# Kernel tuning notes

Measured on AMD Instinct MI355X. Metric: run time of the kernel, lower is better.

The kernel has to match this reference:

```python
import jax, jax.numpy as jnp
import numpy as np

# Module hyperparameters (match init_kwargs)
T0, Z0, T1, Z1, K, S, ROUTING = 4, 16, 8, 16, 5, 1, 3
PAD = 2  # hard-coded padding=2 in the torch module
N, H, W_SP = 4, 128, 128


def setup_inputs() -> dict:
    key = jax.random.key(0)
    k1, k2 = jax.random.split(key)
    u = jax.random.normal(k1, (N, T0, Z0, H, W_SP), dtype=jnp.float32)
    # t_0 independent Conv2d(z_0 -> t_1*z_1, k, s, padding=2, bias=False) weights
    W = jax.random.normal(k2, (T0, T1 * Z1, Z0, K, K), dtype=jnp.float32) * 0.05
    return {"u": u, "W": W}


def _squash(p):
    # squash along last (z_1) axis, matching torch: p_norm = sqrt(|p|^2 + 1e-9)
    n2 = jnp.sum(p * p, axis=-1, keepdims=True)
    n = jnp.sqrt(n2 + 1e-9)
    return n2 / (1.0 + n2) * p / n


def _capsule_convs(u, W):
    # t_0 independent convs == one grouped conv with feature_group_count=t_0
    n, t0, z0, h, w = u.shape
    x = u.reshape(n, t0 * z0, h, w)
    wk = W.reshape(t0 * T1 * Z1, z0, K, K)
    y = jax.lax.conv_general_dilated(
        x, wk, window_strides=(S, S), padding=[(PAD, PAD), (PAD, PAD)],
        dimension_numbers=("NCHW", "OIHW", "NCHW"), feature_group_count=t0)
    h1, w1 = y.shape[2], y.shape[3]
    # [N, t0*t1*z1, H1, W1] -> u_hat [t0, N, H1, W1, t1, z1]
    y = y.reshape(n, t0, T1, Z1, h1, w1)
    return jnp.transpose(y, (1, 0, 4, 5, 2, 3))


def _routing(u_hat):
    t0, n, h, w, t1, z1 = u_hat.shape
    dt = u_hat.dtype
    b = jnp.zeros((t0, n, t1, h, w), dt)  # NCHW layout per capsule type
    neg_inf = jnp.array(-jnp.inf, dt)
    zero = jnp.array(0.0, dt)
    win = (1, 1, 1, K, K)
    ones = (1, 1, 1, 1, 1)
    pad = [(0, 0), (0, 0), (0, 0), (PAD, PAD), (PAD, PAD)]
    v = None
    for d in range(ROUTING):
        uh = jax.lax.stop_gradient(u_hat) if d < ROUTING - 1 else u_hat
        # stability max: max_pool2d(k,1,pad=2) (pads with -inf) then max over t1
        b_max = jax.lax.reduce_window(b, neg_inf, jax.lax.max, win, ones, pad)
        b_max = jnp.max(b_max, axis=2, keepdims=True)
        c = jnp.exp(b - b_max)  # [t0, N, t1, H, W]
        # conv2d_same with ones kernel [1,t1,k,k] == channel-sum then kxk box-sum
        sum_c = jax.lax.reduce_window(jnp.sum(c, axis=2, keepdims=True), zero,
                                      jax.lax.add, win, ones, pad)
        r = c / sum_c                                   # [t0, N, t1, H, W]
        r = jnp.transpose(r, (0, 1, 3, 4, 2))[..., None]  # [t0,N,H,W,t1,1]
        p = jnp.sum(r * uh, axis=0)                     # [N, H, W, t1, z1]
        v = _squash(p)
        # NOTE: the original torch code computes b + (u_hat*v).sum(4) into a
        # list `b_t_list_` that is never assigned back, so b stays zero across
        # iterations. We faithfully reproduce that (no b update).
    return jnp.transpose(v, (0, 3, 4, 1, 2))  # [N, t1, z1, H, W]


def reference(u, W):
    return _routing(_capsule_convs(u, W))
```

## Files before the change

kernel.cpp:

```cpp
#include <hip/hip_runtime.h>
#include <hip/hip_bf16.h>


#define CI 64
#define CO 128
#define HS 128
#define WS 128

typedef __attribute__((ext_vector_type(8))) short bf16x8;
typedef __attribute__((ext_vector_type(4))) float f32x4;


__global__ __launch_bounds__(256) void k_reorder(const float* __restrict__ Wsrc,
                                                 ushort* __restrict__ Wr2) {
    int idx = blockIdx.x * 256 + threadIdx.x;
    if (idx >= 25 * 128 * 64) return;
    int ci = idx & 63;
    int r  = idx >> 6;
    int co = r & 127;
    int kk = r >> 7;
    int t0 = ci >> 4, z0 = ci & 15;
    float v = Wsrc[((t0 * CO + co) * 16 + z0) * 25 + kk];
    __hip_bfloat16 b = __float2bfloat16(v);
    Wr2[idx] = *(ushort*)&b;
}

__global__ __launch_bounds__(256) void k_pre(const float* __restrict__ u,
                                             ushort* __restrict__ ut) {
    __shared__ float lt[64][65];
    int b = blockIdx.x;
    int wc = b & 1; int nh = b >> 1; int h = nh & 127; int n = nh >> 7;
    int w0 = wc * 64;
    int t = threadIdx.x;
    int w = t & 63; int cg = t >> 6;
    const float* up = u + (size_t)n * (CI * HS * WS) + h * WS + w0 + w;
#pragma unroll
    for (int i = 0; i < 16; ++i) {
        int ci = cg * 16 + i;
        lt[w][ci] = up[(size_t)ci * (HS * WS)];
    }
    __syncthreads();
    int ci2 = t & 63; int pg = t >> 6;
    ushort* op = ut + (((size_t)(n * HS + h)) * WS + w0) * 64 + ci2;
#pragma unroll
    for (int i = 0; i < 16; ++i) {
        int w2 = pg * 16 + i;
        __hip_bfloat16 bv = __float2bfloat16(lt[w2][ci2]);
        op[(size_t)w2 * 64] = *(ushort*)&bv;
    }
}

__global__ __launch_bounds__(256) void k_caps(const ushort* __restrict__ ut,
                                              const ushort* __restrict__ Wr2,
                                              float* __restrict__ out) {
    __shared__ ushort As[240 * 64];
    __shared__ ushort Bs[128 * 64];

    int bid = blockIdx.x;
    int bx = bid & 7, by = (bid >> 3) & 15, n = bid >> 7;
    int h0 = by * 8, w0 = bx * 16;
    int tid = threadIdx.x;

    for (int i = tid; i < 1920; i += 256) {
        int p = i >> 3, c = i & 7;
        int rr = p / 20, cc = p - rr * 20;
        int hh = h0 + rr - 2, ww = w0 + cc - 2;
        bf16x8 v = {};
        if ((unsigned)hh < 128u && (unsigned)ww < 128u)
            v = *(const bf16x8*)(ut + (((size_t)(n * HS + hh)) * WS + ww) * 64 + c * 8);
        *(bf16x8*)&As[p * 64 + ((c ^ (p & 7)) << 3)] = v;
    }

    int lane = tid & 63;
    int wid  = tid >> 6;
    int wm4  = (wid >> 1) * 4;
    int wn64 = (wid & 1) * 64;
    int q = lane >> 4, m16 = lane & 15;

    f32x4 acc[4][4] = {};

    bf16x8 pre[4];
#pragma unroll
    for (int j = 0; j < 4; ++j)
        pre[j] = *(const bf16x8*)(Wr2 + (tid + j * 256) * 8);

    for (int kk = 0; kk < 25; ++kk) {
        int kh = kk / 5, kw = kk - kh * 5;
        __syncthreads();
#pragma unroll
        for (int j = 0; j < 4; ++j) {
            int i = tid + j * 256;
            int co = i >> 3, c = i & 7;
            *(bf16x8*)&Bs[co * 64 + ((c ^ (co & 7)) << 3)] = pre[j];
        }
        __syncthreads();
        if (kk < 24) {
#pragma unroll
            for (int j = 0; j < 4; ++j)
                pre[j] = *(const bf16x8*)(Wr2 + (kk + 1) * 8192 + (tid + j * 256) * 8);
        }
#pragma unroll
        for (int ks = 0; ks < 2; ++ks) {
            bf16x8 a[4], bb[4];
#pragma unroll
            for (int mi = 0; mi < 4; ++mi) {
                int p = (wm4 + mi + kh) * 20 + m16 + kw;
                int slot = (ks * 4 + q) ^ (p & 7);
                a[mi] = *(const bf16x8*)&As[p * 64 + slot * 8];
            }
#pragma unroll
            for (int ni = 0; ni < 4; ++ni) {
                int co = wn64 + ni * 16 + m16;
                int slot = (ks * 4 + q) ^ (co & 7);
                bb[ni] = *(const bf16x8*)&Bs[co * 64 + slot * 8];
            }
#pragma unroll
            for (int mi = 0; mi < 4; ++mi)
#pragma unroll
                for (int ni = 0; ni < 4; ++ni)
                    acc[mi][ni] = __builtin_amdgcn_mfma_f32_16x16x32_bf16(
                        a[mi], bb[ni], acc[mi][ni], 0, 0, 0);
        }
    }

#pragma unroll
    for (int mi = 0; mi < 4; ++mi) {
        int h = h0 + wm4 + mi;
        int hlo = h - 2; if (hlo < 0) hlo = 0;
        int hhi = h + 2; if (hhi > 127) hhi = 127;
        float cnth = (float)(hhi - hlo + 1);
#pragma unroll
        for (int ni = 0; ni < 4; ++ni) {
            f32x4 cv = acc[mi][ni];
            float ov[4];
#pragma unroll
            for (int reg = 0; reg < 4; ++reg) {
                int w = w0 + q * 4 + reg;
                int wlo = w - 2; if (wlo < 0) wlo = 0;
                int whi = w + 2; if (whi > 127) whi = 127;
                float s = 1.f / (8.f * cnth * (float)(whi - wlo + 1));
                float pv = cv[reg] * s;
                float n2 = pv * pv;
                n2 += __shfl_xor(n2, 1);
                n2 += __shfl_xor(n2, 2);
                n2 += __shfl_xor(n2, 4);
                n2 += __shfl_xor(n2, 8);
                float fac = n2 / ((1.f + n2) * sqrtf(n2 + 1e-9f));
                ov[reg] = pv * fac;
            }
            int co = wn64 + ni * 16 + m16;
            float4 st = make_float4(ov[0], ov[1], ov[2], ov[3]);
            *(float4*)(out + (((size_t)(n * CO + co)) << 14) + h * WS + w0 + q * 4) = st;
        }
    }
}

extern "C" void kernel_launch(void* const* d_in, const int* in_sizes, int n_in,
                              void* d_out, int out_size, void* d_ws, size_t ws_size,
                              hipStream_t stream) {
    const float* u    = (const float*)d_in[0];
    const float* Wsrc = (const float*)d_in[1];
    float* out = (float*)d_out;
    ushort* Wr2 = (ushort*)d_ws;
    ushort* ut  = (ushort*)((char*)d_ws + 409600);

    k_reorder<<<800, 256, 0, stream>>>(Wsrc, Wr2);
    k_pre<<<1024, 256, 0, stream>>>(u, ut);
    k_caps<<<512, 256, 0, stream>>>(ut, Wr2, out);
}
```

Measured before the change: 114.7 us.

## Fuse input transpose into conv kernel and stream weights from global memory

Removes the separate k_pre transpose kernel. The conv kernel now loads fp32 NCHW input directly, converts it to bf16 and writes it into a padded shared-memory halo tile (stride 80 to avoid bank conflicts). Tiles grow to 16x16 pixels per 512-thread block, with each wave computing 8 rows by 32 output channels. Weight fragments are read straight from global/L2 into registers with one-step prefetch, replacing the per-tap shared-memory staging and its two barriers. The trade-offs are fewer blocks (256), scalar strided LDS writes during the halo load, and more redundant halo reads of fp32 input.

```diff
diff --git a/kernel.cpp b/kernel.cpp
--- a/kernel.cpp
+++ b/kernel.cpp
@@ -4,12 +4,9 @@
 
 #define CI 64
 #define CO 128
-#define HS 128
-#define WS 128
 
 typedef __attribute__((ext_vector_type(8))) short bf16x8;
 typedef __attribute__((ext_vector_type(4))) float f32x4;
-
 
 __global__ __launch_bounds__(256) void k_reorder(const float* __restrict__ Wsrc,
                                                  ushort* __restrict__ Wr2) {
@@ -20,117 +17,100 @@
     int co = r & 127;
     int kk = r >> 7;
     int t0 = ci >> 4, z0 = ci & 15;
-    float v = Wsrc[((t0 * CO + co) * 16 + z0) * 25 + kk];
-    __hip_bfloat16 b = __float2bfloat16(v);
+    __hip_bfloat16 b = __float2bfloat16(Wsrc[((t0 * CO + co) * 16 + z0) * 25 + kk]);
     Wr2[idx] = *(ushort*)&b;
 }
 
-__global__ __launch_bounds__(256) void k_pre(const float* __restrict__ u,
-                                             ushort* __restrict__ ut) {
-    __shared__ float lt[64][65];
-    int b = blockIdx.x;
-    int wc = b & 1; int nh = b >> 1; int h = nh & 127; int n = nh >> 7;
-    int w0 = wc * 64;
-    int t = threadIdx.x;
-    int w = t & 63; int cg = t >> 6;
-    const float* up = u + (size_t)n * (CI * HS * WS) + h * WS + w0 + w;
+__global__ __launch_bounds__(512) void k_caps(const float* __restrict__ u,
+                                              const ushort* __restrict__ Wr2,
+                                              float* __restrict__ out) {
+    __shared__ ushort As[400 * 80];
+
+    int tid = threadIdx.x;
+    int bid = blockIdx.x;
+    int bx = bid & 7, by = (bid >> 3) & 7, n = bid >> 6;
+    int h0 = by * 16, w0 = bx * 16;
+
+    const float* ub = u + (size_t)n * (CI * 128 * 128);
+
 #pragma unroll
-    for (int i = 0; i < 16; ++i) {
-        int ci = cg * 16 + i;
-        lt[w][ci] = up[(size_t)ci * (HS * WS)];
+    for (int j = 0; j < 3; ++j) {
+        int P = tid + j * 512;
+        if (P < 1280) {
+            int rr = P >> 6, ci = P & 63;
+            int hh = h0 + rr - 2;
+            bool rok = (unsigned)hh < 128u;
+            const float* src = ub + (((size_t)ci << 7) + hh) * 128 + (w0 - 4);
+            float4 ch[6];
+#pragma unroll
+            for (int k = 0; k < 6; ++k) {
+                int wc = w0 - 4 + k * 4;
+                ch[k] = (rok && (unsigned)wc < 128u)
+                            ? *(const float4*)(src + k * 4)
+                            : make_float4(0.f, 0.f, 0.f, 0.f);
+            }
+#pragma unroll
+            for (int k = 0; k < 6; ++k) {
+                float vals[4] = {ch[k].x, ch[k].y, ch[k].z, ch[k].w};
+#pragma unroll
+                for (int e = 0; e < 4; ++e) {
+                    int cc = k * 4 + e - 2;
+                    if ((unsigned)cc < 20u) {
+                        __hip_bfloat16 bv = __float2bfloat16(vals[e]);
+                        As[(rr * 20 + cc) * 80 + ci] = *(ushort*)&bv;
+                    }
+                }
+            }
+        }
     }
     __syncthreads();
-    int ci2 = t & 63; int pg = t >> 6;
-    ushort* op = ut + (((size_t)(n * HS + h)) * WS + w0) * 64 + ci2;
-#pragma unroll
-    for (int i = 0; i < 16; ++i) {
-        int w2 = pg * 16 + i;
-        __hip_bfloat16 bv = __float2bfloat16(lt[w2][ci2]);
-        op[(size_t)w2 * 64] = *(ushort*)&bv;
-    }
-}
 
-__global__ __launch_bounds__(256) void k_caps(const ushort* __restrict__ ut,
-                                              const ushort* __restrict__ Wr2,
-                                              float* __restrict__ out) {
-    __shared__ ushort As[240 * 64];
-    __shared__ ushort Bs[128 * 64];
-
-    int bid = blockIdx.x;
-    int bx = bid & 7, by = (bid >> 3) & 15, n = bid >> 7;
-    int h0 = by * 8, w0 = bx * 16;
-    int tid = threadIdx.x;
-
-    for (int i = tid; i < 1920; i += 256) {
-        int p = i >> 3, c = i & 7;
-        int rr = p / 20, cc = p - rr * 20;
-        int hh = h0 + rr - 2, ww = w0 + cc - 2;
-        bf16x8 v = {};
-        if ((unsigned)hh < 128u && (unsigned)ww < 128u)
-            v = *(const bf16x8*)(ut + (((size_t)(n * HS + hh)) * WS + ww) * 64 + c * 8);
-        *(bf16x8*)&As[p * 64 + ((c ^ (p & 7)) << 3)] = v;
-    }
-
-    int lane = tid & 63;
-    int wid  = tid >> 6;
-    int wm4  = (wid >> 1) * 4;
-    int wn64 = (wid & 1) * 64;
+    int lane = tid & 63, wid = tid >> 6;
+    int wm = wid >> 2;
+    int wn = wid & 3;
     int q = lane >> 4, m16 = lane & 15;
 
-    f32x4 acc[4][4] = {};
+    f32x4 acc[8][2] = {};
 
-    bf16x8 pre[4];
+    int aBase = (wm * 160 + m16) * 80 + q * 8;
+
+    const ushort* bp = Wr2 + (wn * 32 + m16) * 64 + q * 8;
+    bf16x8 bnxt0 = *(const bf16x8*)bp;
+    bf16x8 bnxt1 = *(const bf16x8*)(bp + 1024);
+
+    int soff = 0, kw = 0;
+    for (int step = 0; step < 50; ++step) {
+        int ks = step & 1;
+        bf16x8 b0 = bnxt0, b1 = bnxt1;
+        bp += ks ? (8192 - 32) : 32;
+        if (step < 49) {
+            bnxt0 = *(const bf16x8*)bp;
+            bnxt1 = *(const bf16x8*)(bp + 1024);
+        }
+        int au = aBase + soff + ks * 32;
+        bf16x8 a[8];
 #pragma unroll
-    for (int j = 0; j < 4; ++j)
-        pre[j] = *(const bf16x8*)(Wr2 + (tid + j * 256) * 8);
-
-    for (int kk = 0; kk < 25; ++kk) {
-        int kh = kk / 5, kw = kk - kh * 5;
-        __syncthreads();
+        for (int mi = 0; mi < 8; ++mi)
+            a[mi] = *(const bf16x8*)(As + au + mi * 1600);
 #pragma unroll
-        for (int j = 0; j < 4; ++j) {
-            int i = tid + j * 256;
-            int co = i >> 3, c = i & 7;
-            *(bf16x8*)&Bs[co * 64 + ((c ^ (co & 7)) << 3)] = pre[j];
+        for (int mi = 0; mi < 8; ++mi) {
+            acc[mi][0] = __builtin_amdgcn_mfma_f32_16x16x32_bf16(a[mi], b0, acc[mi][0], 0, 0, 0);
+            acc[mi][1] = __builtin_amdgcn_mfma_f32_16x16x32_bf16(a[mi], b1, acc[mi][1], 0, 0, 0);
         }
-        __syncthreads();
-        if (kk < 24) {
-#pragma unroll
-            for (int j = 0; j < 4; ++j)
-                pre[j] = *(const bf16x8*)(Wr2 + (kk + 1) * 8192 + (tid + j * 256) * 8);
-        }
-#pragma unroll
-        for (int ks = 0; ks < 2; ++ks) {
-            bf16x8 a[4], bb[4];
-#pragma unroll
-            for (int mi = 0; mi < 4; ++mi) {
-                int p = (wm4 + mi + kh) * 20 + m16 + kw;
-                int slot = (ks * 4 + q) ^ (p & 7);
-                a[mi] = *(const bf16x8*)&As[p * 64 + slot * 8];
-            }
-#pragma unroll
-            for (int ni = 0; ni < 4; ++ni) {
-                int co = wn64 + ni * 16 + m16;
-                int slot = (ks * 4 + q) ^ (co & 7);
-                bb[ni] = *(const bf16x8*)&Bs[co * 64 + slot * 8];
-            }
-#pragma unroll
-            for (int mi = 0; mi < 4; ++mi)
-#pragma unroll
-                for (int ni = 0; ni < 4; ++ni)
-                    acc[mi][ni] = __builtin_amdgcn_mfma_f32_16x16x32_bf16(
-                        a[mi], bb[ni], acc[mi][ni], 0, 0, 0);
+        if (ks) {
+            if (kw < 4) { kw++; soff += 80; }
+            else        { kw = 0; soff += 1280; }
         }
     }
 
 #pragma unroll
-    for (int mi = 0; mi < 4; ++mi) {
-        int h = h0 + wm4 + mi;
+    for (int mi = 0; mi < 8; ++mi) {
+        int h = h0 + wm * 8 + mi;
         int hlo = h - 2; if (hlo < 0) hlo = 0;
         int hhi = h + 2; if (hhi > 127) hhi = 127;
         float cnth = (float)(hhi - hlo + 1);
 #pragma unroll
-        for (int ni = 0; ni < 4; ++ni) {
+        for (int ni = 0; ni < 2; ++ni) {
             f32x4 cv = acc[mi][ni];
             float ov[4];
 #pragma unroll
@@ -148,9 +128,9 @@
                 float fac = n2 / ((1.f + n2) * sqrtf(n2 + 1e-9f));
                 ov[reg] = pv * fac;
             }
-            int co = wn64 + ni * 16 + m16;
-            float4 st = make_float4(ov[0], ov[1], ov[2], ov[3]);
-            *(float4*)(out + (((size_t)(n * CO + co)) << 14) + h * WS + w0 + q * 4) = st;
+            int co = wn * 32 + ni * 16 + m16;
+            *(float4*)(out + (((size_t)(n * CO + co)) << 14) + h * 128 + w0 + q * 4) =
+                make_float4(ov[0], ov[1], ov[2], ov[3]);
         }
     }
 }
@@ -162,9 +142,7 @@
     const float* Wsrc = (const float*)d_in[1];
     float* out = (float*)d_out;
     ushort* Wr2 = (ushort*)d_ws;
-    ushort* ut  = (ushort*)((char*)d_ws + 409600);
 
     k_reorder<<<800, 256, 0, stream>>>(Wsrc, Wr2);
-    k_pre<<<1024, 256, 0, stream>>>(u, ut);
-    k_caps<<<512, 256, 0, stream>>>(ut, Wr2, out);
+    k_caps<<<256, 512, 0, stream>>>(u, Wr2, out);
 }
```

Result: slower. 118.5 us (+3.3%).
